# Kernel optimization log

Measured on AMD Instinct MI355X. Metric: run time of the kernel, lower is better.

## Reference

```python
import jax, jax.numpy as jnp
import numpy as np

B, N = 128, 1024

def setup_inputs() -> dict:
    key = jax.random.key(0)
    k1, k2 = jax.random.split(key)
    probs = jax.random.uniform(k1, (B, N), dtype=jnp.float32)
    co_matrix = jax.random.uniform(k2, (N, N), dtype=jnp.float32)
    return {"probs": probs, "co_matrix": co_matrix}

def reference(probs, co_matrix):
    # diff[b, i, j] = probs[b, j] - probs[b, i]
    diff = probs[:, None, :] - probs[:, :, None]          # [B, N, N]
    weighted = jnp.square(diff) * co_matrix[None, :, :]   # [B, N, N]
    eps = 1e-8
    n_pos = jnp.sum((co_matrix > 0).astype(jnp.float32))
    # sum over (i, j) of mean over batch
    loss = jnp.sum(jnp.mean(weighted, axis=0)) / (n_pos + eps)
    return loss
```

## Files before the change

kernel.cpp:

```cpp
#include <hip/hip_runtime.h>


#define B_DIM 128
#define N_DIM 1024
#define PAD 136

typedef __bf16 bf16x8 __attribute__((ext_vector_type(8)));
typedef float  f32x4  __attribute__((ext_vector_type(4)));

static __device__ inline unsigned short f2bf(float f) {
    union { float f; unsigned u; } v; v.f = f;
    return (unsigned short)((v.u + 0x7fffu + ((v.u >> 16) & 1u)) >> 16);
}
static __device__ inline float bf2f(unsigned short h) {
    union { unsigned u; float f; } v; v.u = ((unsigned)h) << 16;
    return v.f;
}

__global__ __launch_bounds__(256) void tile_kernel(const float* __restrict__ P,
                                                   const float* __restrict__ C,
                                                   float* __restrict__ psum,
                                                   unsigned* __restrict__ pcnt) {
    __shared__ unsigned short PT[64][PAD];
    __shared__ float ts[64];
    __shared__ float wsum[4];
    __shared__ unsigned wcnt[4];

    const int tid = threadIdx.x, bid = blockIdx.x;
    const int l = tid & 63, w = tid >> 6;
    const int i0 = (bid >> 5) * 32, j0 = (bid & 31) * 32;
    const int wr = w >> 1, wc = w & 1;

    const int gcol = j0 + wc * 16 + (l & 15);
    float cv0 = C[(i0 + wr * 16 + (l >> 4) * 4 + 0) * N_DIM + gcol];
    float cv1 = C[(i0 + wr * 16 + (l >> 4) * 4 + 1) * N_DIM + gcol];
    float cv2 = C[(i0 + wr * 16 + (l >> 4) * 4 + 2) * N_DIM + gcol];
    float cv3 = C[(i0 + wr * 16 + (l >> 4) * 4 + 3) * N_DIM + gcol];

    const float4* P4 = (const float4*)P;
#pragma unroll
    for (int r = 0; r < 8; ++r) {
        const int pan = (r < 4) ? 0 : 1;
        const int p0  = (r < 4) ? i0 : j0;
        const int b   = (r & 3) * 32 + (tid >> 3);
        const int q   = tid & 7;
        float4 v = P4[b * (N_DIM / 4) + (p0 >> 2) + q];
        PT[pan * 32 + q * 4 + 0][b] = f2bf(v.x);
        PT[pan * 32 + q * 4 + 1][b] = f2bf(v.y);
        PT[pan * 32 + q * 4 + 2][b] = f2bf(v.z);
        PT[pan * 32 + q * 4 + 3][b] = f2bf(v.w);
    }
    __syncthreads();

    if (tid < 64) {
        float s = 0.f;
#pragma unroll 8
        for (int b = 0; b < B_DIM; ++b) {
            float v = bf2f(PT[tid][b]);
            s = fmaf(v, v, s);
        }
        ts[tid] = s;
    }

    f32x4 acc = {0.f, 0.f, 0.f, 0.f};
    const int ar = wr * 16 + (l & 15);
    const int br = 32 + wc * 16 + (l & 15);
    const int ko = (l >> 4) * 8;
#pragma unroll
    for (int s = 0; s < 4; ++s) {
        bf16x8 af = *(const bf16x8*)&PT[ar][s * 32 + ko];
        bf16x8 bf = *(const bf16x8*)&PT[br][s * 32 + ko];
        acc = __builtin_amdgcn_mfma_f32_16x16x32_bf16(af, bf, acc, 0, 0, 0);
    }
    __syncthreads();

    const float tj = ts[32 + wc * 16 + (l & 15)];
    float loss = 0.f;
    unsigned cnt = 0;
    {
        const int rb = wr * 16 + (l >> 4) * 4;
        loss = fmaf(cv0, ts[rb + 0] + tj - 2.f * acc[0], loss);
        loss = fmaf(cv1, ts[rb + 1] + tj - 2.f * acc[1], loss);
        loss = fmaf(cv2, ts[rb + 2] + tj - 2.f * acc[2], loss);
        loss = fmaf(cv3, ts[rb + 3] + tj - 2.f * acc[3], loss);
        cnt = (cv0 > 0.f) + (cv1 > 0.f) + (cv2 > 0.f) + (cv3 > 0.f);
    }
#pragma unroll
    for (int off = 32; off > 0; off >>= 1) {
        loss += __shfl_down(loss, off);
        cnt  += __shfl_down(cnt, off);
    }
    if (l == 0) { wsum[w] = loss; wcnt[w] = cnt; }
    __syncthreads();
    if (tid == 0) {
        psum[bid] = wsum[0] + wsum[1] + wsum[2] + wsum[3];
        pcnt[bid] = wcnt[0] + wcnt[1] + wcnt[2] + wcnt[3];
    }
}

__global__ __launch_bounds__(256) void reduce_kernel(const float* __restrict__ psum,
                                                     const unsigned* __restrict__ pcnt,
                                                     float* __restrict__ out) {
    __shared__ double ws_[4];
    __shared__ unsigned wc_[4];
    const int tid = threadIdx.x;
    double s = 0.0; unsigned c = 0;
#pragma unroll
    for (int r = 0; r < 4; ++r) {
        s += (double)psum[r * 256 + tid];
        c += pcnt[r * 256 + tid];
    }
#pragma unroll
    for (int off = 32; off > 0; off >>= 1) {
        s += __shfl_down(s, off);
        c += __shfl_down(c, off);
    }
    const int wave = tid >> 6, lane = tid & 63;
    if (lane == 0) { ws_[wave] = s; wc_[wave] = c; }
    __syncthreads();
    if (tid == 0) {
        double st = ws_[0] + ws_[1] + ws_[2] + ws_[3];
        double ct = (double)(wc_[0] + wc_[1] + wc_[2] + wc_[3]);
        out[0] = (float)(st / ((double)B_DIM * (ct + 1e-8)));
    }
}

extern "C" void kernel_launch(void* const* d_in, const int* in_sizes, int n_in,
                              void* d_out, int out_size, void* d_ws, size_t ws_size,
                              hipStream_t stream) {
    const float* probs = (const float*)d_in[0];
    const float* co    = (const float*)d_in[1];
    float* out = (float*)d_out;

    float*    psum = (float*)d_ws;
    unsigned* pcnt = (unsigned*)((char*)d_ws + 4096);

    tile_kernel<<<1024, 256, 0, stream>>>(probs, co, psum, pcnt);
    reduce_kernel<<<1, 256, 0, stream>>>(psum, pcnt, out);
}
```

Before: 62.09 us.

## Exploit symmetry of squared differences to process only upper-triangular tiles

```diff
diff --git a/kernel.cpp b/kernel.cpp
--- a/kernel.cpp
+++ b/kernel.cpp
@@ -4,6 +4,7 @@
 #define B_DIM 128
 #define N_DIM 1024
 #define PAD 136
+#define NBLK 528
 
 typedef __bf16 bf16x8 __attribute__((ext_vector_type(8)));
 typedef float  f32x4  __attribute__((ext_vector_type(4)));
@@ -28,14 +29,23 @@
 
     const int tid = threadIdx.x, bid = blockIdx.x;
     const int l = tid & 63, w = tid >> 6;
-    const int i0 = (bid >> 5) * 32, j0 = (bid & 31) * 32;
+
+    int ti = 0, rem = bid, rowlen = 32;
+    while (rem >= rowlen) { rem -= rowlen; --rowlen; ++ti; }
+    const int tj = ti + rem;
+    const int i0 = ti * 32, j0 = tj * 32;
+    const bool offdiag = (ti != tj);
+
     const int wr = w >> 1, wc = w & 1;
 
     const int gcol = j0 + wc * 16 + (l & 15);
-    float cv0 = C[(i0 + wr * 16 + (l >> 4) * 4 + 0) * N_DIM + gcol];
-    float cv1 = C[(i0 + wr * 16 + (l >> 4) * 4 + 1) * N_DIM + gcol];
-    float cv2 = C[(i0 + wr * 16 + (l >> 4) * 4 + 2) * N_DIM + gcol];
-    float cv3 = C[(i0 + wr * 16 + (l >> 4) * 4 + 3) * N_DIM + gcol];
+    const int grow = i0 + wr * 16 + (l >> 4) * 4;
+    float cv0 = C[(grow + 0) * N_DIM + gcol];
+    float cv1 = C[(grow + 1) * N_DIM + gcol];
+    float cv2 = C[(grow + 2) * N_DIM + gcol];
+    float cv3 = C[(grow + 3) * N_DIM + gcol];
+    f32x4 cvT = {0.f, 0.f, 0.f, 0.f};
+    if (offdiag) cvT = *(const f32x4*)&C[(size_t)gcol * N_DIM + grow];
 
     const float4* P4 = (const float4*)P;
 #pragma unroll
@@ -74,17 +84,27 @@
     }
     __syncthreads();
 
-    const float tj = ts[32 + wc * 16 + (l & 15)];
+    const float tjc = ts[32 + wc * 16 + (l & 15)];
+    const int rb = wr * 16 + (l >> 4) * 4;
+    float w0 = ts[rb + 0] + tjc - 2.f * acc[0];
+    float w1 = ts[rb + 1] + tjc - 2.f * acc[1];
+    float w2 = ts[rb + 2] + tjc - 2.f * acc[2];
+    float w3 = ts[rb + 3] + tjc - 2.f * acc[3];
     float loss = 0.f;
-    unsigned cnt = 0;
-    {
-        const int rb = wr * 16 + (l >> 4) * 4;
-        loss = fmaf(cv0, ts[rb + 0] + tj - 2.f * acc[0], loss);
-        loss = fmaf(cv1, ts[rb + 1] + tj - 2.f * acc[1], loss);
-        loss = fmaf(cv2, ts[rb + 2] + tj - 2.f * acc[2], loss);
-        loss = fmaf(cv3, ts[rb + 3] + tj - 2.f * acc[3], loss);
-        cnt = (cv0 > 0.f) + (cv1 > 0.f) + (cv2 > 0.f) + (cv3 > 0.f);
+    unsigned cnt = (cv0 > 0.f) + (cv1 > 0.f) + (cv2 > 0.f) + (cv3 > 0.f);
+    if (offdiag) {
+        loss = fmaf(cv0 + cvT[0], w0, loss);
+        loss = fmaf(cv1 + cvT[1], w1, loss);
+        loss = fmaf(cv2 + cvT[2], w2, loss);
+        loss = fmaf(cv3 + cvT[3], w3, loss);
+        cnt += (cvT[0] > 0.f) + (cvT[1] > 0.f) + (cvT[2] > 0.f) + (cvT[3] > 0.f);
+    } else {
+        loss = fmaf(cv0, w0, loss);
+        loss = fmaf(cv1, w1, loss);
+        loss = fmaf(cv2, w2, loss);
+        loss = fmaf(cv3, w3, loss);
     }
+
 #pragma unroll
     for (int off = 32; off > 0; off >>= 1) {
         loss += __shfl_down(loss, off);
@@ -104,12 +124,9 @@
     __shared__ double ws_[4];
     __shared__ unsigned wc_[4];
     const int tid = threadIdx.x;
-    double s = 0.0; unsigned c = 0;
-#pragma unroll
-    for (int r = 0; r < 4; ++r) {
-        s += (double)psum[r * 256 + tid];
-        c += pcnt[r * 256 + tid];
-    }
+    double s = (double)psum[tid] + (double)psum[tid + 256];
+    unsigned c = pcnt[tid] + pcnt[tid + 256];
+    if (tid < NBLK - 512) { s += (double)psum[tid + 512]; c += pcnt[tid + 512]; }
 #pragma unroll
     for (int off = 32; off > 0; off >>= 1) {
         s += __shfl_down(s, off);
@@ -133,8 +150,8 @@
     float* out = (float*)d_out;
 
     float*    psum = (float*)d_ws;
-    unsigned* pcnt = (unsigned*)((char*)d_ws + 4096);
+    unsigned* pcnt = (unsigned*)((char*)d_ws + 2112 + 64);
 
-    tile_kernel<<<1024, 256, 0, stream>>>(probs, co, psum, pcnt);
+    tile_kernel<<<NBLK, 256, 0, stream>>>(probs, co, psum, pcnt);
     reduce_kernel<<<1, 256, 0, stream>>>(psum, pcnt, out);
 }
```

Result: no change. 61.76 us (-0.5%).
